# Kernel tuning notes

Hardware: AMD Instinct MI355X
Metric: run time of the kernel (lower is better)

## Reference

```python
import jax, jax.numpy as jnp
import numpy as np

TOPK = 2

def setup_inputs() -> dict:
    key = jax.random.key(0)
    ks = jax.random.split(key, 5)
    B, S, D, H, E = 2, 4096, 1024, 2048, 8
    x = jax.random.normal(ks[0], (B, S, D), dtype=jnp.float32)
    router_w = jax.random.normal(ks[1], (E, D), dtype=jnp.float32) * 0.02
    w1 = jax.random.normal(ks[2], (E, D, H), dtype=jnp.float32) * 0.02
    w3 = jax.random.normal(ks[3], (E, D, H), dtype=jnp.float32) * 0.02
    w2 = jax.random.normal(ks[4], (E, H, D), dtype=jnp.float32) * 0.02
    return {"x": x, "router_w": router_w, "w1": w1, "w3": w3, "w2": w2}

def reference(x, router_w, w1, w3, w2):
    B, S, D = x.shape
    E = router_w.shape[0]
    xf = x.reshape(-1, D)                      # [T, D]
    T = xf.shape[0]
    logits = (xf @ router_w.T).astype(jnp.float32)      # [T, E]
    weights, indices = jax.lax.top_k(logits, TOPK)      # [T, k]
    weights = jax.nn.softmax(weights, axis=-1).astype(x.dtype)
    prob = jax.nn.softmax(logits, axis=-1)              # [T, E] fp32
    P = prob.mean(axis=0).astype(x.dtype)               # [E]
    mask = jnp.zeros((T, E), jnp.float32).at[jnp.arange(T)[:, None], indices].set(1.0)
    f = mask.mean(axis=0).astype(x.dtype)               # [E]
    aux_loss = E * jnp.sum(f * P)
    out = jnp.zeros_like(xf)
    for e in range(E):
        # combine weight for expert e per token (0 if not routed here)
        coef = jnp.sum(jnp.where(indices == e, weights, jnp.zeros_like(weights)), axis=-1)  # [T]
        h = jax.nn.silu(xf @ w1[e]) * (xf @ w3[e])      # [T, H] SwiGLU
        out = out + coef[:, None] * (h @ w2[e])         # masked combine == gather/scatter
    return out.reshape(B, S, D), aux_loss
```

## Files before the change

kernel.cpp:

```cpp
#include <hip/hip_runtime.h>
#include <hip/hip_bf16.h>

#define TT 8192
#define DD 1024
#define HH 2048
#define EE 8

typedef __bf16 bf16x8 __attribute__((ext_vector_type(8)));
typedef float floatx4 __attribute__((ext_vector_type(4)));
typedef short shortx8 __attribute__((ext_vector_type(8)));

__device__ __forceinline__ short f2bf(float f) {
  unsigned u = __float_as_uint(f);
  u += 0x7fffu + ((u >> 16) & 1u);
  return (short)(u >> 16);
}

__device__ __forceinline__ float bf2f(short s) {
  return __uint_as_float(((unsigned)(unsigned short)s) << 16);
}

__device__ __forceinline__ void gld16(const void* g, void* l) {
  __builtin_amdgcn_global_load_lds((const __attribute__((address_space(1))) void*)g,
                                   (__attribute__((address_space(3))) void*)l, 16, 0, 0);
}

__global__ __launch_bounds__(256) void router_kernel(
    const float* __restrict__ x, const float* __restrict__ rw,
    int* __restrict__ cpad, float* __restrict__ ppad,
    int* __restrict__ list_token, float* __restrict__ list_coef,
    int* __restrict__ tokpk, float* __restrict__ tokcf,
    short* __restrict__ xb)
{
  __shared__ int   sE0[32], sE1[32], lcnt[EE], sbase[EE], lp0[32], lp1[32];
  __shared__ float sG0[32], sG1[32], sP[EE];
  const int tid = threadIdx.x;
  if (tid < EE) { sP[tid] = 0.f; lcnt[tid] = 0; }
  __syncthreads();
  const int lane = tid & 63, wv = tid >> 6;
  const int t0 = blockIdx.x * 32;
  for (int ti = 0; ti < 8; ++ti) {
    const int s = wv * 8 + ti;
    const int t = t0 + s;
    float sc[EE];
#pragma unroll
    for (int e = 0; e < EE; ++e) sc[e] = 0.f;
#pragma unroll
    for (int j = 0; j < 4; ++j) {
      float4 xv = *(const float4*)(x + (size_t)t * DD + j * 256 + lane * 4);
#pragma unroll
      for (int e = 0; e < EE; ++e) {
        float4 rv = *(const float4*)(rw + e * DD + j * 256 + lane * 4);
        sc[e] += xv.x * rv.x + xv.y * rv.y + xv.z * rv.z + xv.w * rv.w;
      }
      if (xb) {
        short4 sv = make_short4(f2bf(xv.x), f2bf(xv.y), f2bf(xv.z), f2bf(xv.w));
        *(short4*)(xb + (size_t)t * DD + j * 256 + lane * 4) = sv;
      }
    }
#pragma unroll
    for (int off = 32; off > 0; off >>= 1)
#pragma unroll
      for (int e = 0; e < EE; ++e)
        sc[e] += __shfl_down(sc[e], off);
    if (lane == 0) {
      int i0 = 0; float l0 = sc[0];
      for (int e = 1; e < EE; ++e) if (sc[e] > l0) { l0 = sc[e]; i0 = e; }
      int i1 = -1; float l1 = -3.4e38f;
      for (int e = 0; e < EE; ++e) if (e != i0 && sc[e] > l1) { l1 = sc[e]; i1 = e; }
      const float g0 = 1.f / (1.f + __expf(l1 - l0));
      float pr[EE]; float sum = 0.f;
      for (int e = 0; e < EE; ++e) { pr[e] = __expf(sc[e] - l0); sum += pr[e]; }
      const float inv = 1.f / sum;
      for (int e = 0; e < EE; ++e) atomicAdd(&sP[e], pr[e] * inv);
      sE0[s] = i0; sE1[s] = i1; sG0[s] = g0; sG1[s] = 1.f - g0;
    }
  }
  __syncthreads();
  if (tid < 32) {
    lp0[tid] = atomicAdd(&lcnt[sE0[tid]], 1);
    lp1[tid] = atomicAdd(&lcnt[sE1[tid]], 1);
  }
  __syncthreads();
  if (tid < EE) {
    sbase[tid] = atomicAdd(&cpad[tid * 16], lcnt[tid]);
    atomicAdd(&ppad[tid * 16], sP[tid]);
  }
  __syncthreads();
  if (tid < 32) {
    int e0 = sE0[tid], e1 = sE1[tid], t = t0 + tid;
    int p0 = sbase[e0] + lp0[tid];
    int p1 = sbase[e1] + lp1[tid];
    list_token[e0 * TT + p0] = t; list_coef[e0 * TT + p0] = sG0[tid];
    list_token[e1 * TT + p1] = t; list_coef[e1 * TT + p1] = sG1[tid];
    tokpk[t * 2]     = (e0 << 13) | p0;  tokcf[t * 2]     = sG0[tid];
    tokpk[t * 2 + 1] = (e1 << 13) | p1;  tokcf[t * 2 + 1] = sG1[tid];
  }
}

__global__ void aux_kernel(const int* __restrict__ cpad, const float* __restrict__ ppad,
                           int* __restrict__ offsets, float* __restrict__ out_aux)
{
  if (threadIdx.x == 0) {
    float aux = 0.f; int off = 0;
    for (int e = 0; e < EE; ++e) {
      aux += ((float)cpad[e * 16] / (float)TT) * (ppad[e * 16] / (float)TT);
      offsets[e] = off; off += cpad[e * 16];
    }
    *out_aux = aux * (float)EE;
  }
}

__global__ __launch_bounds__(256) void convt13_kernel(const float* __restrict__ w1,
                                                      const float* __restrict__ w3,
                                                      short* __restrict__ out)
{
  __shared__ short T[64 * 74];
  const int t = threadIdx.x;
  const int z = blockIdx.z;
  const int is3 = (z >= EE) ? 1 : 0;
  const int e = is3 ? (z - EE) : z;
  const float* in = (is3 ? w3 : w1) + (size_t)e * DD * HH;
  short* o = out + (size_t)e * DD * HH * 2;
  const int c0 = blockIdx.x * 64, r0 = blockIdx.y * 64;
#pragma unroll
  for (int p = 0; p < 4; ++p) {
    int r = p * 16 + (t >> 4), c4 = (t & 15) * 4;
    float4 v = *(const float4*)(in + (size_t)(r0 + r) * HH + c0 + c4);
    short4 s = make_short4(f2bf(v.x), f2bf(v.y), f2bf(v.z), f2bf(v.w));
    *(short4*)&T[r * 74 + c4] = s;
  }
  __syncthreads();
#pragma unroll
  for (int q = 0; q < 2; ++q) {
    int u = q * 256 + t;
    int oc = u >> 3, k8 = (u & 7) * 8;
    shortx8 s;
#pragma unroll
    for (int j = 0; j < 8; ++j) s[j] = T[(k8 + j) * 74 + oc];
    int c = c0 + oc;
    int grow = 2 * (c & ~31) + (c & 31) + (is3 ? 32 : 0);
    *(shortx8*)&o[(size_t)grow * DD + r0 + k8] = s;
  }
}

__global__ __launch_bounds__(256) void convt_kernel(const float* __restrict__ in, short* __restrict__ out,
                                                    int R, int C)
{
  __shared__ short T[64 * 74];
  const int t = threadIdx.x;
  in  += (size_t)blockIdx.z * R * C;
  out += (size_t)blockIdx.z * R * C;
  const int c0 = blockIdx.x * 64, r0 = blockIdx.y * 64;
#pragma unroll
  for (int p = 0; p < 4; ++p) {
    int r = p * 16 + (t >> 4), c4 = (t & 15) * 4;
    float4 v = *(const float4*)(in + (size_t)(r0 + r) * C + c0 + c4);
    short4 s = make_short4(f2bf(v.x), f2bf(v.y), f2bf(v.z), f2bf(v.w));
    *(short4*)&T[r * 74 + c4] = s;
  }
  __syncthreads();
#pragma unroll
  for (int q = 0; q < 2; ++q) {
    int u = q * 256 + t;
    int oc = u >> 3, k8 = (u & 7) * 8;
    shortx8 s;
#pragma unroll
    for (int j = 0; j < 8; ++j) s[j] = T[(k8 + j) * 74 + oc];
    *(shortx8*)&out[(size_t)(c0 + oc) * R + r0 + k8] = s;
  }
}


#define PH_BAR()  { __builtin_amdgcn_s_barrier(); __builtin_amdgcn_sched_barrier(0); }
#define WAITL0()  { asm volatile("s_waitcnt lgkmcnt(0)" ::: "memory"); __builtin_amdgcn_sched_barrier(0); }
#define WAITVN(n) { asm volatile("s_waitcnt vmcnt(" #n ")" ::: "memory"); __builtin_amdgcn_sched_barrier(0); }

template<int NT>
__device__ __forceinline__ void mma_core(char* SM, int tid,
    const char* a00, const char* a01, const char* a10, const char* a11,
    const char* b00, const char* b01, const char* b10, const char* b11,
    floatx4 (&acc)[8][4])
{
  const int lane = tid & 63, w = tid >> 6;
  const int l16 = lane & 15, quad = lane >> 4;
  const int wm = (w >> 2) & 1, wn = w & 3;
  const int cx = (((l16 >> 1) & 1) << 4) | (((l16 >> 2) & 1) << 5) | ((l16 & 1) << 6);
  const int ck0 = (quad * 16) ^ cx;
  const int arb = (wm * 128 + l16) * 128;
  const int brb = 32768 + (wn * 64 + l16) * 128;
  const int wq = w * 2048;

#define SA_(u,h,p0,p1) { gld16((p0) + (size_t)(u) * 128, SM + (((u) & 1) << 16) + (h) * 16384 + wq); \
                         gld16((p1) + (size_t)(u) * 128, SM + (((u) & 1) << 16) + (h) * 16384 + wq + 1024); }
#define SB_(u,h,p0,p1) { gld16((p0) + (size_t)(u) * 128, SM + (((u) & 1) << 16) + 32768 + (h) * 16384 + wq); \
                         gld16((p1) + (size_t)(u) * 128, SM + (((u) & 1) << 16) + 32768 + (h) * 16384 + wq + 1024); }
#define LA_(mi) { a[mi][0] = *(const bf16x8*)(SM + cur + arb + (mi) * 2048 + ck0); \
                  a[mi][1] = *(const bf16x8*)(SM + cur + arb + (mi) * 2048 + (ck0 ^ 64)); }
#define LB_(ni) { b[ni][0] = *(const bf16x8*)(SM + cur + brb + (ni) * 2048 + ck0); \
                  b[ni][1] = *(const bf16x8*)(SM + cur + brb + (ni) * 2048 + (ck0 ^ 64)); }
#define MM_(mi,ni) { acc[mi][ni] = __builtin_amdgcn_mfma_f32_16x16x32_bf16(a[mi][0], b[ni][0], acc[mi][ni], 0, 0, 0); \
                     acc[mi][ni] = __builtin_amdgcn_mfma_f32_16x16x32_bf16(a[mi][1], b[ni][1], acc[mi][ni], 0, 0, 0); }

  SA_(0, 0, a00, a01); SA_(0, 1, a10, a11);
  SB_(0, 0, b00, b01); SB_(0, 1, b10, b11);
  SA_(1, 0, a00, a01); SA_(1, 1, a10, a11);
  WAITVN(4);
  __builtin_amdgcn_s_barrier();
  __builtin_amdgcn_sched_barrier(0);

#pragma unroll 2
  for (int t = 0; t < NT; ++t) {
    const int cur = (t & 1) << 16;
    bf16x8 a[8][2], b[4][2];
    LA_(0) LA_(1) LA_(2) LA_(3) LB_(0) LB_(1)
    if (t + 1 < NT) SB_(t + 1, 0, b00, b01);
    PH_BAR(); WAITL0();
    __builtin_amdgcn_s_setprio(1);
    MM_(0,0) MM_(1,0) MM_(2,0) MM_(3,0) MM_(0,1) MM_(1,1) MM_(2,1) MM_(3,1)
    __builtin_amdgcn_s_setprio(0);
    PH_BAR();
    LA_(4) LA_(5) LA_(6) LA_(7) LB_(2) LB_(3)
    if (t + 1 < NT) SB_(t + 1, 1, b10, b11);
    PH_BAR(); WAITL0();
    __builtin_amdgcn_s_setprio(1);
    MM_(4,2) MM_(5,2) MM_(6,2) MM_(7,2) MM_(4,3) MM_(5,3) MM_(6,3) MM_(7,3)
    __builtin_amdgcn_s_setprio(0);
    PH_BAR();
    if (t + 2 < NT) SA_(t + 2, 0, a00, a01);
    PH_BAR();
    __builtin_amdgcn_s_setprio(1);
    MM_(0,2) MM_(1,2) MM_(2,2) MM_(3,2) MM_(0,3) MM_(1,3) MM_(2,3) MM_(3,3)
    __builtin_amdgcn_s_setprio(0);
    PH_BAR();
    if (t + 2 < NT) SA_(t + 2, 1, a10, a11);
    PH_BAR();
    __builtin_amdgcn_s_setprio(1);
    MM_(4,0) MM_(5,0) MM_(6,0) MM_(7,0) MM_(4,1) MM_(5,1) MM_(6,1) MM_(7,1)
    __builtin_amdgcn_s_setprio(0);
    if (t + 2 < NT) { WAITVN(4); } else { WAITVN(0); }
    PH_BAR();
  }
#undef SA_
#undef SB_
#undef LA_
#undef LB_
#undef MM_
}

__global__ __launch_bounds__(512, 2) void g1p_kernel(
    const short* __restrict__ xb, const short* __restrict__ w13t,
    const int* __restrict__ cpad, const int* __restrict__ offsets,
    const int* __restrict__ list_token, short* __restrict__ Hbuf)
{
  const int lin = blockIdx.x + 16 * (blockIdx.y + 32 * blockIdx.z);
  const int xcd = lin & 7, c = lin >> 3;
  const int e = c >> 6, rb = (c >> 1) & 31, nb = (xcd << 1) | (c & 1);
  const int cnt = cpad[e * 16];
  if (rb * 256 >= cnt) return;
  __shared__ char SM[131072];
  const int tid = threadIdx.x;
  const int lane = tid & 63, w = tid >> 6;
  const int srow = lane >> 3;
  const int scol = (((lane ^ (lane >> 4)) & 1) << 4)
                 | ((((lane >> 1) ^ (lane >> 5)) & 1) << 5)
                 | ((((lane >> 2) ^ (lane >> 3)) & 1) << 6);
  const int* lt = list_token + e * TT;
  const char* ap[2][2];
#pragma unroll
  for (int h = 0; h < 2; ++h)
#pragma unroll
    for (int i = 0; i < 2; ++i) {
      int gr = rb * 256 + h * 128 + (w * 2 + i) * 8 + srow;
      int tok = (gr < cnt) ? lt[gr] : lt[0];
      ap[h][i] = (const char*)xb + (size_t)tok * 2048 + scol;
    }
  const char* bb = (const char*)w13t + ((size_t)e * 4096 + nb * 256) * 2048
                 + (size_t)(w * 16 + srow) * 2048 + scol;
  floatx4 acc[8][4] = {};
  mma_core<16>(SM, tid, ap[0][0], ap[0][1], ap[1][0], ap[1][1],
               bb, bb + 8 * 2048, bb + 128 * 2048, bb + 136 * 2048, acc);
  const int off = offsets[e];
  const int l16 = lane & 15, quad = lane >> 4;
  const int wm = (w >> 2) & 1, wn = w & 3;
#pragma unroll
  for (int mi = 0; mi < 8; ++mi)
#pragma unroll
    for (int r = 0; r < 4; ++r) {
      int grow = rb * 256 + wm * 128 + mi * 16 + quad * 4 + r;
      if (grow < cnt) {
        size_t rowbase = (size_t)(off + grow) * HH + nb * 128 + wn * 32;
#pragma unroll
        for (int ni = 0; ni < 2; ++ni) {
          float aa = acc[mi][ni][r], bbv = acc[mi][ni + 2][r];
          float hv = aa / (1.f + __expf(-aa)) * bbv;
          Hbuf[rowbase + ni * 16 + l16] = f2bf(hv);
        }
      }
    }
}

__global__ __launch_bounds__(512, 2) void g2q_kernel(
    const short* __restrict__ Hbuf, const short* __restrict__ w2t,
    const int* __restrict__ cpad, const int* __restrict__ offsets,
    short* __restrict__ Obuf)
{
  const int nb = blockIdx.x, rb = blockIdx.y, e = blockIdx.z;
  const int cnt = cpad[e * 16];
  if (rb * 256 >= cnt) return;
  __shared__ char SM[131072];
  const int tid = threadIdx.x;
  const int lane = tid & 63, w = tid >> 6;
  const int srow = lane >> 3;
  const int scol = (((lane ^ (lane >> 4)) & 1) << 4)
                 | ((((lane >> 1) ^ (lane >> 5)) & 1) << 5)
                 | ((((lane >> 2) ^ (lane >> 3)) & 1) << 6);
  const int off = offsets[e];
  const char* ap[2][2];
#pragma unroll
  for (int h = 0; h < 2; ++h)
#pragma unroll
    for (int i = 0; i < 2; ++i) {
      int gr = rb * 256 + h * 128 + (w * 2 + i) * 8 + srow;
      int cg = (gr < cnt) ? gr : (cnt - 1);
      ap[h][i] = (const char*)Hbuf + (size_t)(off + cg) * 4096 + scol;
    }
  const char* bb = (const char*)w2t + ((size_t)e * DD + nb * 256) * 4096
                 + (size_t)(w * 16 + srow) * 4096 + scol;
  floatx4 acc[8][4] = {};
  mma_core<32>(SM, tid, ap[0][0], ap[0][1], ap[1][0], ap[1][1],
               bb, bb + 8 * 4096, bb + 128 * 4096, bb + 136 * 4096, acc);
  const int l16 = lane & 15, quad = lane >> 4;
  const int wm = (w >> 2) & 1, wn = w & 3;
#pragma unroll
  for (int mi = 0; mi < 8; ++mi)
#pragma unroll
    for (int r = 0; r < 4; ++r) {
      int grow = rb * 256 + wm * 128 + mi * 16 + quad * 4 + r;
      if (grow < cnt) {
        short* orow = Obuf + (size_t)(off + grow) * DD + nb * 256 + wn * 64;
#pragma unroll
        for (int ni = 0; ni < 4; ++ni)
          orow[ni * 16 + l16] = f2bf(acc[mi][ni][r]);
      }
    }
}

__global__ __launch_bounds__(256) void combine_kernel(
    const short* __restrict__ Obuf, const int* __restrict__ offsets,
    const int* __restrict__ tokpk, const float* __restrict__ tokcf,
    float* __restrict__ out)
{
  const int tid = threadIdx.x, lane = tid & 63, wv = tid >> 6;
  const int t = blockIdx.x * 4 + wv;
  const int pk0 = tokpk[t * 2], pk1 = tokpk[t * 2 + 1];
  const float c0 = tokcf[t * 2], c1 = tokcf[t * 2 + 1];
  const size_t r0 = (size_t)(offsets[pk0 >> 13] + (pk0 & 8191)) * DD;
  const size_t r1 = (size_t)(offsets[pk1 >> 13] + (pk1 & 8191)) * DD;
  float* orow = out + (size_t)t * DD;
#pragma unroll
  for (int p = 0; p < 2; ++p) {
    int cidx = p * 512 + lane * 8;
    shortx8 a = *(const shortx8*)(Obuf + r0 + cidx);
    shortx8 b = *(const shortx8*)(Obuf + r1 + cidx);
    float v[8];
#pragma unroll
    for (int j = 0; j < 8; ++j) v[j] = c0 * bf2f(a[j]) + c1 * bf2f(b[j]);
    *(float4*)(orow + cidx)     = make_float4(v[0], v[1], v[2], v[3]);
    *(float4*)(orow + cidx + 4) = make_float4(v[4], v[5], v[6], v[7]);
  }
}

__global__ __launch_bounds__(256, 2) void g1s_kernel(
    const float* __restrict__ x, const float* __restrict__ w1, const float* __restrict__ w3,
    const int* __restrict__ cpad, const int* __restrict__ offsets,
    const int* __restrict__ list_token, short* __restrict__ Hbuf)
{
  const int e = blockIdx.z, rb = blockIdx.y, nb = blockIdx.x;
  const int cnt = cpad[e * 16];
  if (rb * 128 >= cnt) return;
  __shared__ short Asm[128 * 40];
  __shared__ short B1sm[128 * 40];
  __shared__ short B3sm[128 * 40];
  const int tid = threadIdx.x, lane = tid & 63, wv = tid >> 6;
  const int wm = (wv >> 1) * 64, wn = (wv & 1) * 64;
  const int quad = lane >> 4, l16 = lane & 15;
  floatx4 acc1[4][4] = {{{0.f}}};
  floatx4 acc3[4][4] = {{{0.f}}};
  const int ar = tid >> 3, ak = (tid & 7) * 4;
  const int bp = tid & 63, bq = tid >> 6;
  const int bswz = (bq ^ ((bp >> 2) & 3)) * 8;
  const int bo0 = (2 * bp) * 40 + bswz, bo1 = bo0 + 40;
  int aro[4], bro[4];
#pragma unroll
  for (int mi = 0; mi < 4; ++mi) aro[mi] = (wm + mi * 16 + l16) * 40 + quad * 8;
#pragma unroll
  for (int ni = 0; ni < 4; ++ni) {
    int nl = wn + ni * 16 + l16;
    bro[ni] = nl * 40 + ((quad ^ ((nl >> 3) & 3)) * 8);
  }
  int tok[4];
#pragma unroll
  for (int i = 0; i < 4; ++i) {
    int gr = rb * 128 + ar + 32 * i;
    tok[i] = (gr < cnt) ? list_token[e * TT + gr] : list_token[e * TT];
  }
  const float* w1e = w1 + (size_t)e * DD * HH + (size_t)nb * 128;
  const float* w3e = w3 + (size_t)e * DD * HH + (size_t)nb * 128;
  for (int k0 = 0; k0 < DD; k0 += 32) {
    __syncthreads();
#pragma unroll
    for (int i = 0; i < 4; ++i) {
      int r = ar + 32 * i;
      float4 v = *(const float4*)(x + (size_t)tok[i] * DD + k0 + ak);
      short4 sv = make_short4(f2bf(v.x), f2bf(v.y), f2bf(v.z), f2bf(v.w));
      *(short4*)&Asm[r * 40 + ak] = sv;
    }
    {
      float2 u[8];
#pragma unroll
      for (int j = 0; j < 8; ++j) u[j] = *(const float2*)(w1e + (size_t)(k0 + bq * 8 + j) * HH + 2 * bp);
      shortx8 p0, p1;
#pragma unroll
      for (int j = 0; j < 8; ++j) { p0[j] = f2bf(u[j].x); p1[j] = f2bf(u[j].y); }
      *(shortx8*)&B1sm[bo0] = p0; *(shortx8*)&B1sm[bo1] = p1;
    }
    {
      float2 u[8];
#pragma unroll
      for (int j = 0; j < 8; ++j) u[j] = *(const float2*)(w3e + (size_t)(k0 + bq * 8 + j) * HH + 2 * bp);
      shortx8 p0, p1;
#pragma unroll
      for (int j = 0; j < 8; ++j) { p0[j] = f2bf(u[j].x); p1[j] = f2bf(u[j].y); }
      *(shortx8*)&B3sm[bo0] = p0; *(shortx8*)&B3sm[bo1] = p1;
    }
    __syncthreads();
    bf16x8 af[4], b1f[4], b3f[4];
#pragma unroll
    for (int mi = 0; mi < 4; ++mi) af[mi] = *(const bf16x8*)&Asm[aro[mi]];
#pragma unroll
    for (int ni = 0; ni < 4; ++ni) {
      b1f[ni] = *(const bf16x8*)&B1sm[bro[ni]];
      b3f[ni] = *(const bf16x8*)&B3sm[bro[ni]];
    }
#pragma unroll
    for (int mi = 0; mi < 4; ++mi)
#pragma unroll
      for (int ni = 0; ni < 4; ++ni) {
        acc1[mi][ni] = __builtin_amdgcn_mfma_f32_16x16x32_bf16(af[mi], b1f[ni], acc1[mi][ni], 0, 0, 0);
        acc3[mi][ni] = __builtin_amdgcn_mfma_f32_16x16x32_bf16(af[mi], b3f[ni], acc3[mi][ni], 0, 0, 0);
      }
  }
  const int off = offsets[e];
#pragma unroll
  for (int mi = 0; mi < 4; ++mi)
#pragma unroll
    for (int r = 0; r < 4; ++r) {
      int row = wm + mi * 16 + quad * 4 + r;
      int grow = rb * 128 + row;
      if (grow < cnt) {
        size_t rowbase = (size_t)(off + grow) * HH + (size_t)nb * 128 + wn;
#pragma unroll
        for (int ni = 0; ni < 4; ++ni) {
          float a = acc1[mi][ni][r], b = acc3[mi][ni][r];
          float h = a / (1.f + __expf(-a)) * b;
          Hbuf[rowbase + ni * 16 + l16] = f2bf(h);
        }
      }
    }
}

__global__ __launch_bounds__(256, 2) void g2s_kernel(
    const short* __restrict__ Hbuf, const float* __restrict__ w2,
    const int* __restrict__ cpad, const int* __restrict__ offsets,
    const int* __restrict__ list_token, const float* __restrict__ list_coef,
    float* __restrict__ out)
{
  const int e = blockIdx.z, rb = blockIdx.y, nb = blockIdx.x;
  const int cnt = cpad[e * 16];
  if (rb * 128 >= cnt) return;
  __shared__ short Asm[128 * 40];
  __shared__ short Bsm[128 * 40];
  const int tid = threadIdx.x, lane = tid & 63, wv = tid >> 6;
  const int wm = (wv >> 1) * 64, wn = (wv & 1) * 64;
  const int quad = lane >> 4, l16 = lane & 15;
  floatx4 acc[4][4] = {{{0.f}}};
  const int ar = tid >> 3, ak = (tid & 7) * 4;
  const int bp = tid & 63, bq = tid >> 6;
  const int bswz = (bq ^ ((bp >> 2) & 3)) * 8;
  const int bo0 = (2 * bp) * 40 + bswz, bo1 = bo0 + 40;
  int aro[4], bro[4];
#pragma unroll
  for (int mi = 0; mi < 4; ++mi) aro[mi] = (wm + mi * 16 + l16) * 40 + quad * 8;
#pragma unroll
  for (int ni = 0; ni < 4; ++ni) {
    int nl = wn + ni * 16 + l16;
    bro[ni] = nl * 40 + ((quad ^ ((nl >> 3) & 3)) * 8);
  }
  const int off = offsets[e];
  size_t hrow[4];
#pragma unroll
  for (int i = 0; i < 4; ++i) {
    int gr = rb * 128 + ar + 32 * i;
    int cg = (gr < cnt) ? gr : (cnt - 1);
    hrow[i] = (size_t)(off + cg) * HH;
  }
  const float* w2e = w2 + (size_t)e * HH * DD + (size_t)nb * 128;
  for (int k0 = 0; k0 < HH; k0 += 32) {
    __syncthreads();
#pragma unroll
    for (int i = 0; i < 4; ++i) {
      int r = ar + 32 * i;
      short4 sv = *(const short4*)(Hbuf + hrow[i] + k0 + ak);
      *(short4*)&Asm[r * 40 + ak] = sv;
    }
    {
      float2 u[8];
#pragma unroll
      for (int j = 0; j < 8; ++j) u[j] = *(const float2*)(w2e + (size_t)(k0 + bq * 8 + j) * DD + 2 * bp);
      shortx8 p0, p1;
#pragma unroll
      for (int j = 0; j < 8; ++j) { p0[j] = f2bf(u[j].x); p1[j] = f2bf(u[j].y); }
      *(shortx8*)&Bsm[bo0] = p0; *(shortx8*)&Bsm[bo1] = p1;
    }
    __syncthreads();
    bf16x8 af[4], bf[4];
#pragma unroll
    for (int mi = 0; mi < 4; ++mi) af[mi] = *(const bf16x8*)&Asm[aro[mi]];
#pragma unroll
    for (int ni = 0; ni < 4; ++ni) bf[ni] = *(const bf16x8*)&Bsm[bro[ni]];
#pragma unroll
    for (int mi = 0; mi < 4; ++mi)
#pragma unroll
      for (int ni = 0; ni < 4; ++ni)
        acc[mi][ni] = __builtin_amdgcn_mfma_f32_16x16x32_bf16(af[mi], bf[ni], acc[mi][ni], 0, 0, 0);
  }
#pragma unroll
  for (int mi = 0; mi < 4; ++mi)
#pragma unroll
    for (int r = 0; r < 4; ++r) {
      int row = wm + mi * 16 + quad * 4 + r;
      int grow = rb * 128 + row;
      if (grow < cnt) {
        int tokid = list_token[e * TT + grow];
        float coef = list_coef[e * TT + grow];
        float* orow = out + (size_t)tokid * DD + (size_t)nb * 128 + wn;
#pragma unroll
        for (int ni = 0; ni < 4; ++ni)
          atomicAdd(&orow[ni * 16 + l16], coef * acc[mi][ni][r]);
      }
    }
}

extern "C" void kernel_launch(void* const* d_in, const int* in_sizes, int n_in,
                              void* d_out, int out_size, void* d_ws, size_t ws_size,
                              hipStream_t stream)
{
  const float* x  = (const float*)d_in[0];
  const float* rw = (const float*)d_in[1];
  const float* w1 = (const float*)d_in[2];
  const float* w3 = (const float*)d_in[3];
  const float* w2 = (const float*)d_in[4];
  float* out = (float*)d_out;

  char* ws = (char*)d_ws;
  int*   cpad      = (int*)(ws + 0);
  float* ppad      = (float*)(ws + 512);
  int*   offsets   = (int*)(ws + 1024);
  int*   list_tok  = (int*)(ws + 4096);
  float* list_coef = (float*)(ws + 4096 + EE * TT * 4);
  int*   tokpk     = (int*)(ws + 4096 + 2 * EE * TT * 4);
  float* tokcf     = (float*)(ws + 4096 + 2 * EE * TT * 4 + 2 * TT * 4);

  const size_t OFF_W1T = 1u << 20;
  const size_t OFF_W3T = OFF_W1T + ((size_t)EE * DD * HH * 2);
  const size_t OFF_XBF = OFF_W3T + ((size_t)EE * DD * HH * 2);
  const size_t OFF_HB  = OFF_XBF + ((size_t)TT * DD * 2);
  const size_t NEED    = OFF_HB + ((size_t)(2 * TT + 128) * HH * 2);

  hipMemsetAsync(ws, 0, 1024, stream);

  const bool fast = (ws_size >= NEED);
  short* XBF = fast ? (short*)(ws + OFF_XBF) : nullptr;

  router_kernel<<<256, 256, 0, stream>>>(x, rw, cpad, ppad, list_tok, list_coef, tokpk, tokcf, XBF);
  aux_kernel<<<1, 64, 0, stream>>>(cpad, ppad, offsets, out + (size_t)TT * DD);

  if (fast) {
    short* W13T = (short*)(ws + OFF_W1T);
    short* OB   = (short*)(ws + OFF_W1T);
    short* W2T  = (short*)(ws + OFF_W3T);
    short* HB   = (short*)(ws + OFF_HB);
    convt13_kernel<<<dim3(HH / 64, DD / 64, 2 * EE), 256, 0, stream>>>(w1, w3, W13T);
    g1p_kernel<<<dim3(16, 32, EE), 512, 0, stream>>>(XBF, W13T, cpad, offsets, list_tok, HB);
    convt_kernel<<<dim3(DD / 64, HH / 64, EE), 256, 0, stream>>>(w2, W2T, HH, DD);
    g2q_kernel<<<dim3(DD / 256, 32, EE), 512, 0, stream>>>(HB, W2T, cpad, offsets, OB);
    combine_kernel<<<TT / 4, 256, 0, stream>>>(OB, offsets, tokpk, tokcf, out);
  } else {
    hipMemsetAsync(d_out, 0, (size_t)TT * DD * sizeof(float), stream);
    short* HB = (short*)(ws + (1 << 20));
    g1s_kernel<<<dim3(HH / 128, TT / 128, EE), 256, 0, stream>>>(x, w1, w3, cpad, offsets, list_tok, HB);
    g2s_kernel<<<dim3(DD / 128, TT / 128, EE), 256, 0, stream>>>(HB, w2, cpad, offsets, list_tok, list_coef, out);
  }
}
```

Baseline: 592.4 us.

## Fuse router, aux and weight-conversion kernels into one prep launch

Merges the router, aux-loss and w1/w3 transpose-convert kernels into a single prep_kernel. It also folds the w2 conversion in whenever the workspace is large enough to hold a separate W2T buffer. A last-block-done atomic counter replaces the separate aux kernel. The goal is to remove launch gaps and let the small router work overlap with the bandwidth-bound weight conversion. The cost is a larger workspace requirement and a threadfence/atomic completion pattern.

Result: faster. 578.2 us (-2.4%).

```diff
diff --git a/kernel.cpp b/kernel.cpp
--- a/kernel.cpp
+++ b/kernel.cpp
@@ -25,122 +25,147 @@
                                    (__attribute__((address_space(3))) void*)l, 16, 0, 0);
 }
 
-__global__ __launch_bounds__(256) void router_kernel(
+__global__ __launch_bounds__(256) void prep_kernel(
     const float* __restrict__ x, const float* __restrict__ rw,
-    int* __restrict__ cpad, float* __restrict__ ppad,
+    const float* __restrict__ w1, const float* __restrict__ w3, const float* __restrict__ w2,
+    int* __restrict__ cpad, float* __restrict__ ppad, int* __restrict__ ctr,
+    int* __restrict__ offsets, float* __restrict__ out_aux,
     int* __restrict__ list_token, float* __restrict__ list_coef,
     int* __restrict__ tokpk, float* __restrict__ tokcf,
-    short* __restrict__ xb)
-{
+    short* __restrict__ xb, short* __restrict__ w13t, short* __restrict__ w2t)
+{
+  __shared__ short T[64 * 74];
   __shared__ int   sE0[32], sE1[32], lcnt[EE], sbase[EE], lp0[32], lp1[32];
   __shared__ float sG0[32], sG1[32], sP[EE];
+  const int b = blockIdx.x;
   const int tid = threadIdx.x;
-  if (tid < EE) { sP[tid] = 0.f; lcnt[tid] = 0; }
-  __syncthreads();
-  const int lane = tid & 63, wv = tid >> 6;
-  const int t0 = blockIdx.x * 32;
-  for (int ti = 0; ti < 8; ++ti) {
-    const int s = wv * 8 + ti;
-    const int t = t0 + s;
-    float sc[EE];
-#pragma unroll
-    for (int e = 0; e < EE; ++e) sc[e] = 0.f;
-#pragma unroll
-    for (int j = 0; j < 4; ++j) {
-      float4 xv = *(const float4*)(x + (size_t)t * DD + j * 256 + lane * 4);
-#pragma unroll
-      for (int e = 0; e < EE; ++e) {
-        float4 rv = *(const float4*)(rw + e * DD + j * 256 + lane * 4);
-        sc[e] += xv.x * rv.x + xv.y * rv.y + xv.z * rv.z + xv.w * rv.w;
-      }
-      if (xb) {
-        short4 sv = make_short4(f2bf(xv.x), f2bf(xv.y), f2bf(xv.z), f2bf(xv.w));
-        *(short4*)(xb + (size_t)t * DD + j * 256 + lane * 4) = sv;
-      }
-    }
-#pragma unroll
-    for (int off = 32; off > 0; off >>= 1)
-#pragma unroll
-      for (int e = 0; e < EE; ++e)
-        sc[e] += __shfl_down(sc[e], off);
-    if (lane == 0) {
-      int i0 = 0; float l0 = sc[0];
-      for (int e = 1; e < EE; ++e) if (sc[e] > l0) { l0 = sc[e]; i0 = e; }
-      int i1 = -1; float l1 = -3.4e38f;
-      for (int e = 0; e < EE; ++e) if (e != i0 && sc[e] > l1) { l1 = sc[e]; i1 = e; }
-      const float g0 = 1.f / (1.f + __expf(l1 - l0));
-      float pr[EE]; float sum = 0.f;
-      for (int e = 0; e < EE; ++e) { pr[e] = __expf(sc[e] - l0); sum += pr[e]; }
-      const float inv = 1.f / sum;
-      for (int e = 0; e < EE; ++e) atomicAdd(&sP[e], pr[e] * inv);
-      sE0[s] = i0; sE1[s] = i1; sG0[s] = g0; sG1[s] = 1.f - g0;
-    }
-  }
-  __syncthreads();
-  if (tid < 32) {
-    lp0[tid] = atomicAdd(&lcnt[sE0[tid]], 1);
-    lp1[tid] = atomicAdd(&lcnt[sE1[tid]], 1);
-  }
-  __syncthreads();
-  if (tid < EE) {
-    sbase[tid] = atomicAdd(&cpad[tid * 16], lcnt[tid]);
-    atomicAdd(&ppad[tid * 16], sP[tid]);
-  }
-  __syncthreads();
-  if (tid < 32) {
-    int e0 = sE0[tid], e1 = sE1[tid], t = t0 + tid;
-    int p0 = sbase[e0] + lp0[tid];
-    int p1 = sbase[e1] + lp1[tid];
-    list_token[e0 * TT + p0] = t; list_coef[e0 * TT + p0] = sG0[tid];
-    list_token[e1 * TT + p1] = t; list_coef[e1 * TT + p1] = sG1[tid];
-    tokpk[t * 2]     = (e0 << 13) | p0;  tokcf[t * 2]     = sG0[tid];
-    tokpk[t * 2 + 1] = (e1 << 13) | p1;  tokcf[t * 2 + 1] = sG1[tid];
-  }
-}
-
-__global__ void aux_kernel(const int* __restrict__ cpad, const float* __restrict__ ppad,
-                           int* __restrict__ offsets, float* __restrict__ out_aux)
-{
-  if (threadIdx.x == 0) {
-    float aux = 0.f; int off = 0;
-    for (int e = 0; e < EE; ++e) {
-      aux += ((float)cpad[e * 16] / (float)TT) * (ppad[e * 16] / (float)TT);
-      offsets[e] = off; off += cpad[e * 16];
-    }
-    *out_aux = aux * (float)EE;
-  }
-}
-
-__global__ __launch_bounds__(256) void convt13_kernel(const float* __restrict__ w1,
-                                                      const float* __restrict__ w3,
-                                                      short* __restrict__ out)
-{
-  __shared__ short T[64 * 74];
-  const int t = threadIdx.x;
-  const int z = blockIdx.z;
-  const int is3 = (z >= EE) ? 1 : 0;
-  const int e = is3 ? (z - EE) : z;
-  const float* in = (is3 ? w3 : w1) + (size_t)e * DD * HH;
-  short* o = out + (size_t)e * DD * HH * 2;
-  const int c0 = blockIdx.x * 64, r0 = blockIdx.y * 64;
-#pragma unroll
-  for (int p = 0; p < 4; ++p) {
-    int r = p * 16 + (t >> 4), c4 = (t & 15) * 4;
-    float4 v = *(const float4*)(in + (size_t)(r0 + r) * HH + c0 + c4);
-    short4 s = make_short4(f2bf(v.x), f2bf(v.y), f2bf(v.z), f2bf(v.w));
-    *(short4*)&T[r * 74 + c4] = s;
-  }
-  __syncthreads();
-#pragma unroll
-  for (int q = 0; q < 2; ++q) {
-    int u = q * 256 + t;
-    int oc = u >> 3, k8 = (u & 7) * 8;
-    shortx8 s;
-#pragma unroll
-    for (int j = 0; j < 8; ++j) s[j] = T[(k8 + j) * 74 + oc];
-    int c = c0 + oc;
-    int grow = 2 * (c & ~31) + (c & 31) + (is3 ? 32 : 0);
-    *(shortx8*)&o[(size_t)grow * DD + r0 + k8] = s;
+
+  if (b < 256) {
+    if (tid < EE) { sP[tid] = 0.f; lcnt[tid] = 0; }
+    __syncthreads();
+    const int lane = tid & 63, wv = tid >> 6;
+    const int t0 = b * 32;
+    for (int ti = 0; ti < 8; ++ti) {
+      const int s = wv * 8 + ti;
+      const int t = t0 + s;
+      float sc[EE];
+#pragma unroll
+      for (int e = 0; e < EE; ++e) sc[e] = 0.f;
+#pragma unroll
+      for (int j = 0; j < 4; ++j) {
+        float4 xv = *(const float4*)(x + (size_t)t * DD + j * 256 + lane * 4);
+#pragma unroll
+        for (int e = 0; e < EE; ++e) {
+          float4 rv = *(const float4*)(rw + e * DD + j * 256 + lane * 4);
+          sc[e] += xv.x * rv.x + xv.y * rv.y + xv.z * rv.z + xv.w * rv.w;
+        }
+        if (xb) {
+          short4 sv = make_short4(f2bf(xv.x), f2bf(xv.y), f2bf(xv.z), f2bf(xv.w));
+          *(short4*)(xb + (size_t)t * DD + j * 256 + lane * 4) = sv;
+        }
+      }
+#pragma unroll
+      for (int off = 32; off > 0; off >>= 1)
+#pragma unroll
+        for (int e = 0; e < EE; ++e)
+          sc[e] += __shfl_down(sc[e], off);
+      if (lane == 0) {
+        int i0 = 0; float l0 = sc[0];
+        for (int e = 1; e < EE; ++e) if (sc[e] > l0) { l0 = sc[e]; i0 = e; }
+        int i1 = -1; float l1 = -3.4e38f;
+        for (int e = 0; e < EE; ++e) if (e != i0 && sc[e] > l1) { l1 = sc[e]; i1 = e; }
+        const float g0 = 1.f / (1.f + __expf(l1 - l0));
+        float pr[EE]; float sum = 0.f;
+        for (int e = 0; e < EE; ++e) { pr[e] = __expf(sc[e] - l0); sum += pr[e]; }
+        const float inv = 1.f / sum;
+        for (int e = 0; e < EE; ++e) atomicAdd(&sP[e], pr[e] * inv);
+        sE0[s] = i0; sE1[s] = i1; sG0[s] = g0; sG1[s] = 1.f - g0;
+      }
+    }
+    __syncthreads();
+    if (tid < 32) {
+      lp0[tid] = atomicAdd(&lcnt[sE0[tid]], 1);
+      lp1[tid] = atomicAdd(&lcnt[sE1[tid]], 1);
+    }
+    __syncthreads();
+    if (tid < EE) {
+      sbase[tid] = atomicAdd(&cpad[tid * 16], lcnt[tid]);
+      atomicAdd(&ppad[tid * 16], sP[tid]);
+    }
+    __syncthreads();
+    if (tid < 32) {
+      int e0 = sE0[tid], e1 = sE1[tid], t = t0 + tid;
+      int p0 = sbase[e0] + lp0[tid];
+      int p1 = sbase[e1] + lp1[tid];
+      list_token[e0 * TT + p0] = t; list_coef[e0 * TT + p0] = sG0[tid];
+      list_token[e1 * TT + p1] = t; list_coef[e1 * TT + p1] = sG1[tid];
+      tokpk[t * 2]     = (e0 << 13) | p0;  tokcf[t * 2]     = sG0[tid];
+      tokpk[t * 2 + 1] = (e1 << 13) | p1;  tokcf[t * 2 + 1] = sG1[tid];
+    }
+    __syncthreads();
+    if (tid == 0) {
+      __threadfence();
+      if (atomicAdd(ctr, 1) == 255) {
+        float aux = 0.f; int off = 0;
+        for (int e = 0; e < EE; ++e) {
+          int c   = atomicAdd(&cpad[e * 16], 0);
+          float p = atomicAdd(&ppad[e * 16], 0.f);
+          aux += ((float)c / (float)TT) * (p / (float)TT);
+          offsets[e] = off; off += c;
+        }
+        *out_aux = aux * (float)EE;
+      }
+    }
+  } else if (b < 256 + 8192) {
+    const int u = b - 256;
+    const int xx = u & 31, yy = (u >> 5) & 15, z = u >> 9;
+    const int is3 = (z >= EE) ? 1 : 0;
+    const int e = is3 ? (z - EE) : z;
+    const float* in = (is3 ? w3 : w1) + (size_t)e * DD * HH;
+    short* o = w13t + (size_t)e * DD * HH * 2;
+    const int c0 = xx * 64, r0 = yy * 64;
+#pragma unroll
+    for (int p = 0; p < 4; ++p) {
+      int r = p * 16 + (tid >> 4), c4 = (tid & 15) * 4;
+      float4 v = *(const float4*)(in + (size_t)(r0 + r) * HH + c0 + c4);
+      short4 s = make_short4(f2bf(v.x), f2bf(v.y), f2bf(v.z), f2bf(v.w));
+      *(short4*)&T[r * 74 + c4] = s;
+    }
+    __syncthreads();
+#pragma unroll
+    for (int q = 0; q < 2; ++q) {
+      int uu = q * 256 + tid;
+      int oc = uu >> 3, k8 = (uu & 7) * 8;
+      shortx8 s;
+#pragma unroll
+      for (int j = 0; j < 8; ++j) s[j] = T[(k8 + j) * 74 + oc];
+      int c = c0 + oc;
+      int grow = 2 * (c & ~31) + (c & 31) + (is3 ? 32 : 0);
+      *(shortx8*)&o[(size_t)grow * DD + r0 + k8] = s;
+    }
+  } else {
+    const int v = b - 256 - 8192;
+    const int xx = v & 15, yy = (v >> 4) & 31, z = v >> 9;
+    const float* in = w2 + (size_t)z * HH * DD;
+    short* o = w2t + (size_t)z * HH * DD;
+    const int c0 = xx * 64, r0 = yy * 64;
+#pragma unroll
+    for (int p = 0; p < 4; ++p) {
+      int r = p * 16 + (tid >> 4), c4 = (tid & 15) * 4;
+      float4 vv = *(const float4*)(in + (size_t)(r0 + r) * DD + c0 + c4);
+      short4 s = make_short4(f2bf(vv.x), f2bf(vv.y), f2bf(vv.z), f2bf(vv.w));
+      *(short4*)&T[r * 74 + c4] = s;
+    }
+    __syncthreads();
+#pragma unroll
+    for (int q = 0; q < 2; ++q) {
+      int uu = q * 256 + tid;
+      int oc = uu >> 3, k8 = (uu & 7) * 8;
+      shortx8 s;
+#pragma unroll
+      for (int j = 0; j < 8; ++j) s[j] = T[(k8 + j) * 74 + oc];
+      *(shortx8*)&o[(size_t)(c0 + oc) * HH + r0 + k8] = s;
+    }
   }
 }
 
@@ -567,6 +592,7 @@
   int*   cpad      = (int*)(ws + 0);
   float* ppad      = (float*)(ws + 512);
   int*   offsets   = (int*)(ws + 1024);
+  int*   ctr       = (int*)(ws + 2048);
   int*   list_tok  = (int*)(ws + 4096);
   float* list_coef = (float*)(ws + 4096 + EE * TT * 4);
   int*   tokpk     = (int*)(ws + 4096 + 2 * EE * TT * 4);
@@ -577,28 +603,35 @@
   const size_t OFF_XBF = OFF_W3T + ((size_t)EE * DD * HH * 2);
   const size_t OFF_HB  = OFF_XBF + ((size_t)TT * DD * 2);
   const size_t NEED    = OFF_HB + ((size_t)(2 * TT + 128) * HH * 2);
-
-  hipMemsetAsync(ws, 0, 1024, stream);
-
-  const bool fast = (ws_size >= NEED);
+  const size_t OFF_W2T = NEED;
+  const size_t NEED2   = NEED + ((size_t)EE * DD * HH * 2);
+
+  hipMemsetAsync(ws, 0, 4096, stream);
+
+  const bool fast  = (ws_size >= NEED);
+  const bool tier2 = (ws_size >= NEED2);
   short* XBF = fast ? (short*)(ws + OFF_XBF) : nullptr;
-
-  router_kernel<<<256, 256, 0, stream>>>(x, rw, cpad, ppad, list_tok, list_coef, tokpk, tokcf, XBF);
-  aux_kernel<<<1, 64, 0, stream>>>(cpad, ppad, offsets, out + (size_t)TT * DD);
 
   if (fast) {
     short* W13T = (short*)(ws + OFF_W1T);
     short* OB   = (short*)(ws + OFF_W1T);
-    short* W2T  = (short*)(ws + OFF_W3T);
+    short* W2T  = tier2 ? (short*)(ws + OFF_W2T) : (short*)(ws + OFF_W3T);
     short* HB   = (short*)(ws + OFF_HB);
-    convt13_kernel<<<dim3(HH / 64, DD / 64, 2 * EE), 256, 0, stream>>>(w1, w3, W13T);
+    const int nblk = 256 + 8192 + (tier2 ? 4096 : 0);
+    prep_kernel<<<nblk, 256, 0, stream>>>(x, rw, w1, w3, w2, cpad, ppad, ctr, offsets,
+                                          out + (size_t)TT * DD, list_tok, list_coef,
+                                          tokpk, tokcf, XBF, W13T, W2T);
     g1p_kernel<<<dim3(16, 32, EE), 512, 0, stream>>>(XBF, W13T, cpad, offsets, list_tok, HB);
-    convt_kernel<<<dim3(DD / 64, HH / 64, EE), 256, 0, stream>>>(w2, W2T, HH, DD);
+    if (!tier2)
+      convt_kernel<<<dim3(DD / 64, HH / 64, EE), 256, 0, stream>>>(w2, W2T, HH, DD);
     g2q_kernel<<<dim3(DD / 256, 32, EE), 512, 0, stream>>>(HB, W2T, cpad, offsets, OB);
     combine_kernel<<<TT / 4, 256, 0, stream>>>(OB, offsets, tokpk, tokcf, out);
   } else {
     hipMemsetAsync(d_out, 0, (size_t)TT * DD * sizeof(float), stream);
     short* HB = (short*)(ws + (1 << 20));
+    prep_kernel<<<256, 256, 0, stream>>>(x, rw, w1, w3, w2, cpad, ppad, ctr, offsets,
+                                         out + (size_t)TT * DD, list_tok, list_coef,
+                                         tokpk, tokcf, nullptr, nullptr, nullptr);
     g1s_kernel<<<dim3(HH / 128, TT / 128, EE), 256, 0, stream>>>(x, w1, w3, cpad, offsets, list_tok, HB);
     g2s_kernel<<<dim3(DD / 128, TT / 128, EE), 256, 0, stream>>>(HB, w2, cpad, offsets, list_tok, list_coef, out);
   }
```
